# Performance work log

Measured on AMD Instinct MI355X. Metric: run time of the kernel, lower is better.

## Reference

```python
import jax, jax.numpy as jnp
import numpy as np

D_MODEL = 1024
N_HEADS = 16


def setup_inputs() -> dict:
    key = jax.random.key(0)
    ks = jax.random.split(key, 11)
    B, S, D = 2, 2048, D_MODEL
    scale = 1.0 / np.sqrt(D)
    inp = {
        "q": jax.random.normal(ks[0], (B, S, D), jnp.float32),
        "k": jax.random.normal(ks[1], (B, S, D), jnp.float32),
        "v": jax.random.normal(ks[2], (B, S, D), jnp.float32),
        "W_q": jax.random.normal(ks[3], (D, D), jnp.float32) * scale,
        "b_q": jnp.zeros((D,), jnp.float32),
        "W_k": jax.random.normal(ks[4], (D, D), jnp.float32) * scale,
        "b_k": jnp.zeros((D,), jnp.float32),
        "W_v": jax.random.normal(ks[5], (D, D), jnp.float32) * scale,
        "b_v": jnp.zeros((D,), jnp.float32),
        "W_o": jax.random.normal(ks[6], (D, D), jnp.float32) * scale,
        "b_o": jnp.zeros((D,), jnp.float32),
    }
    return inp


def reference(q, k, v, W_q, b_q, W_k, b_k, W_v, b_v, W_o, b_o):
    B, S, D = q.shape
    H = N_HEADS
    d_k = D // H
    # linear projections, then split heads: [B, H, S, d_k]
    def proj(x, W, b):
        y = jnp.einsum("bsd,de->bse", x, W.T) + b
        return y.reshape(B, S, H, d_k).transpose(0, 2, 1, 3)
    Q = proj(q, W_q, b_q)
    K = proj(k, W_k, b_k)
    V = proj(v, W_v, b_v)
    # scaled dot-product attention with explicit [B,H,S,S] scores
    scores = jnp.einsum("bhqd,bhkd->bhqk", Q, K) / jnp.sqrt(jnp.float32(d_k))
    attn = jax.nn.softmax(scores, axis=-1)
    out = jnp.einsum("bhqk,bhkd->bhqd", attn, V)
    out = out.transpose(0, 2, 1, 3).reshape(B, S, D)
    return jnp.einsum("bsd,de->bse", out, W_o.T) + b_o
```

## Files before the change

### kernel.cpp

```cpp
#include <hip/hip_runtime.h>
#include <hip/hip_bf16.h>
#include <math.h>

typedef __bf16 bf16_t;
typedef bf16_t bf16x8 __attribute__((ext_vector_type(8)));
typedef float f32x4 __attribute__((ext_vector_type(4)));

#define D_MODEL 1024
#define NH 16
#define DK 64
#define SEQ 2048
#define MROWS 4096
#define LDP 72
#define LDSW 64
#define LDC 136

__device__ __forceinline__ bf16x8 ldfrag(const bf16_t* p) {
    union { uint4 u; bf16x8 v; } c;
    c.u = *reinterpret_cast<const uint4*>(p);
    return c.v;
}

__device__ __forceinline__ f32x4 zero4() { f32x4 z = {0.f, 0.f, 0.f, 0.f}; return z; }

__device__ __forceinline__ void gll16(const bf16_t* g, bf16_t* l) {
    __builtin_amdgcn_global_load_lds(
        (const __attribute__((address_space(1))) unsigned int*)g,
        (__attribute__((address_space(3))) unsigned int*)l,
        16, 0, 0);
}

__global__ void pack3(const float* __restrict__ a, const float* __restrict__ b,
                      const float* __restrict__ c,
                      bf16_t* __restrict__ da, bf16_t* __restrict__ db, bf16_t* __restrict__ dc) {
    const float* s = (blockIdx.y == 0) ? a : (blockIdx.y == 1) ? b : c;
    bf16_t* d      = (blockIdx.y == 0) ? da : (blockIdx.y == 1) ? db : dc;
    int i = (blockIdx.x * blockDim.x + threadIdx.x) * 4;
    float4 f = *reinterpret_cast<const float4*>(s + i);
    union { bf16_t h[4]; uint2 u; } o;
    o.h[0] = (bf16_t)f.x; o.h[1] = (bf16_t)f.y; o.h[2] = (bf16_t)f.z; o.h[3] = (bf16_t)f.w;
    *reinterpret_cast<uint2*>(d + i) = o.u;
}

__global__ void pack4(const float* __restrict__ a, const float* __restrict__ b,
                      const float* __restrict__ c, const float* __restrict__ e,
                      bf16_t* __restrict__ da, bf16_t* __restrict__ db,
                      bf16_t* __restrict__ dc, bf16_t* __restrict__ de) {
    const float* s = (blockIdx.y == 0) ? a : (blockIdx.y == 1) ? b : (blockIdx.y == 2) ? c : e;
    bf16_t* d      = (blockIdx.y == 0) ? da : (blockIdx.y == 1) ? db : (blockIdx.y == 2) ? dc : de;
    int i = (blockIdx.x * blockDim.x + threadIdx.x) * 4;
    float4 f = *reinterpret_cast<const float4*>(s + i);
    union { bf16_t h[4]; uint2 u; } o;
    o.h[0] = (bf16_t)f.x; o.h[1] = (bf16_t)f.y; o.h[2] = (bf16_t)f.z; o.h[3] = (bf16_t)f.w;
    *reinterpret_cast<uint2*>(d + i) = o.u;
}

__device__ __forceinline__ void gemm_core(
    const bf16_t* __restrict__ A, const bf16_t* __restrict__ Bm,
    int K, int m0, int n0,
    bf16_t* As, bf16_t* Bs,
    f32x4 acc[4][4]) {

    const int tid = threadIdx.x;
    const int lane = tid & 63;
    const int wid = tid >> 6;
    const int wm = (wid >> 1) * 64, wn = (wid & 1) * 64;
    const int l15 = lane & 15, quad = lane >> 4;

    const int lrow   = lane >> 3;
    const int gcol   = ((lane & 7) ^ lrow) * 8;

    #pragma unroll
    for (int i = 0; i < 4; i++)
        #pragma unroll
        for (int j = 0; j < 4; j++) acc[i][j] = zero4();

    for (int k0 = 0; k0 < K; k0 += 64) {
        __syncthreads();
        #pragma unroll
        for (int t = 0; t < 4; t++) {
            const int rbase = wid * 32 + t * 8;
            gll16(A  + (size_t)(m0 + rbase + lrow) * K + k0 + gcol, As + rbase * LDSW);
            gll16(Bm + (size_t)(n0 + rbase + lrow) * K + k0 + gcol, Bs + rbase * LDSW);
        }
        __syncthreads();
        #pragma unroll
        for (int c = 0; c < 2; c++) {
            bf16x8 af[4], bfr[4];
            #pragma unroll
            for (int i = 0; i < 4; i++) {
                const int row = wm + i * 16 + l15;
                const int pc = ((c * 4 + quad) ^ (l15 & 7)) * 8;
                af[i] = ldfrag(As + row * LDSW + pc);
            }
            #pragma unroll
            for (int j = 0; j < 4; j++) {
                const int row = wn + j * 16 + l15;
                const int pc = ((c * 4 + quad) ^ (l15 & 7)) * 8;
                bfr[j] = ldfrag(Bs + row * LDSW + pc);
            }
            #pragma unroll
            for (int i = 0; i < 4; i++)
                #pragma unroll
                for (int j = 0; j < 4; j++)
                    acc[i][j] = __builtin_amdgcn_mfma_f32_16x16x32_bf16(af[i], bfr[j], acc[i][j], 0, 0, 0);
        }
    }
}

__global__ __launch_bounds__(256, 2) void proj_gemm(
    const bf16_t* __restrict__ qb, const bf16_t* __restrict__ kb,
    const bf16_t* __restrict__ vb,
    const bf16_t* __restrict__ Wq, const bf16_t* __restrict__ Wk,
    const bf16_t* __restrict__ Wv,
    const float* __restrict__ bq, const float* __restrict__ bk, const float* __restrict__ bv,
    bf16_t* __restrict__ Qh, bf16_t* __restrict__ Kh, bf16_t* __restrict__ Vt) {

    __shared__ __align__(16) bf16_t sm[128 * LDC];
    bf16_t* As = sm;
    bf16_t* Bs = sm + 128 * LDSW;
    bf16_t (*Cs)[LDC] = reinterpret_cast<bf16_t(*)[LDC]>(sm);
    f32x4 acc[4][4];

    const int mode = blockIdx.z;
    const bf16_t* X = (mode == 0) ? qb : (mode == 1) ? kb : vb;
    const bf16_t* W = (mode == 0) ? Wq : (mode == 1) ? Wk : Wv;
    const float* bias = (mode == 0) ? bq : (mode == 1) ? bk : bv;
    const int m0 = blockIdx.y * 128, n0 = blockIdx.x * 128;

    gemm_core(X, W, D_MODEL, m0, n0, As, Bs, acc);

    const int tid = threadIdx.x, lane = tid & 63, wid = tid >> 6;
    const int wm = (wid >> 1) * 64, wn = (wid & 1) * 64;
    const int l15 = lane & 15, quad = lane >> 4;

    __syncthreads();
    if (mode != 2) {
        const float sc = (mode == 0) ? 0.125f * 1.44269504f : 1.0f;
        #pragma unroll
        for (int i = 0; i < 4; i++)
            #pragma unroll
            for (int j = 0; j < 4; j++)
                #pragma unroll
                for (int r = 0; r < 4; r++) {
                    int gn = n0 + wn + j * 16 + l15;
                    Cs[wm + i * 16 + quad * 4 + r][wn + j * 16 + l15] =
                        (bf16_t)((acc[i][j][r] + bias[gn]) * sc);
                }
    } else {
        #pragma unroll
        for (int i = 0; i < 4; i++)
            #pragma unroll
            for (int j = 0; j < 4; j++)
                #pragma unroll
                for (int r = 0; r < 4; r++) {
                    int gn = n0 + wn + j * 16 + l15;
                    Cs[wn + j * 16 + l15][wm + i * 16 + quad * 4 + r] =
                        (bf16_t)(acc[i][j][r] + bias[gn]);
                }
    }
    __syncthreads();

    #pragma unroll
    for (int c = tid; c < 2048; c += 256) {
        int row = c >> 4, col8 = (c & 15) << 3;
        uint4 val = *reinterpret_cast<const uint4*>(&Cs[row][col8]);
        if (mode != 2) {
            int gm = m0 + row, gn = n0 + col8;
            int b = gm >> 11, seq = gm & 2047;
            int h = gn >> 6, dk = gn & 63;
            bf16_t* dst = (mode == 0) ? Qh : Kh;
            *reinterpret_cast<uint4*>(dst + ((size_t)(b * NH + h) * SEQ + seq) * DK + dk) = val;
        } else {
            int gn = n0 + row, gm = m0 + col8;
            int b = gm >> 11, seq = gm & 2047;
            int h = gn >> 6, dk = gn & 63;
            *reinterpret_cast<uint4*>(Vt + ((size_t)(b * NH + h) * DK + dk) * SEQ + seq) = val;
        }
    }
}

__global__ __launch_bounds__(256, 2) void out_gemm(
    const bf16_t* __restrict__ Oc, const bf16_t* __restrict__ Wo,
    const float* __restrict__ bo, float* __restrict__ Cout) {

    __shared__ __align__(16) bf16_t As[128 * LDSW];
    __shared__ __align__(16) bf16_t Bs[128 * LDSW];
    f32x4 acc[4][4];
    const int m0 = blockIdx.y * 128, n0 = blockIdx.x * 128;

    gemm_core(Oc, Wo, D_MODEL, m0, n0, As, Bs, acc);

    const int tid = threadIdx.x, lane = tid & 63, wid = tid >> 6;
    const int wm = (wid >> 1) * 64, wn = (wid & 1) * 64;
    const int l15 = lane & 15, quad = lane >> 4;

    #pragma unroll
    for (int i = 0; i < 4; i++)
        #pragma unroll
        for (int j = 0; j < 4; j++)
            #pragma unroll
            for (int r = 0; r < 4; r++) {
                int gm = m0 + wm + i * 16 + quad * 4 + r;
                int gn = n0 + wn + j * 16 + l15;
                Cout[(size_t)gm * D_MODEL + gn] = acc[i][j][r] + bo[gn];
            }
}

__global__ __launch_bounds__(256) void attn_kernel(
    const bf16_t* __restrict__ Qh, const bf16_t* __restrict__ Kh,
    const bf16_t* __restrict__ Vt, bf16_t* __restrict__ Oc) {

    __shared__ __align__(16) bf16_t Ks[64 * LDSW];
    __shared__ __align__(16) bf16_t Vts[64 * LDSW];
    __shared__ __align__(16) bf16_t Pls[64][LDP];

    const int tid = threadIdx.x, lane = tid & 63, wid = tid >> 6;
    const int l15 = lane & 15, quad = lane >> 4;
    const int bh = blockIdx.x;
    const int q0 = blockIdx.y * 64;
    const bf16_t* Qbase = Qh + (size_t)bh * SEQ * DK;
    const bf16_t* Kbase = Kh + (size_t)bh * SEQ * DK;
    const bf16_t* Vbase = Vt + (size_t)bh * DK * SEQ;

    const int lrow = lane >> 3;
    const int gcol = ((lane & 7) ^ lrow) * 8;

    bf16x8 aQ[2];
    #pragma unroll
    for (int c = 0; c < 2; c++)
        aQ[c] = ldfrag(Qbase + (size_t)(q0 + wid * 16 + l15) * DK + c * 32 + quad * 8);

    f32x4 oacc[4];
    #pragma unroll
    for (int j = 0; j < 4; j++) oacc[j] = zero4();
    float l_i[4] = {0.f, 0.f, 0.f, 0.f};

    for (int kt = 0; kt < SEQ / 64; kt++) {
        const int k0 = kt * 64;
        __syncthreads();
        #pragma unroll
        for (int t = 0; t < 2; t++) {
            const int rbase = wid * 16 + t * 8;
            gll16(Kbase + (size_t)(k0 + rbase + lrow) * DK + gcol,  Ks  + rbase * LDSW);
            gll16(Vbase + (size_t)(rbase + lrow) * SEQ + k0 + gcol, Vts + rbase * LDSW);
        }
        __syncthreads();

        f32x4 sacc[4];
        #pragma unroll
        for (int j = 0; j < 4; j++) sacc[j] = zero4();
        #pragma unroll
        for (int c = 0; c < 2; c++) {
            bf16x8 bk4[4];
            #pragma unroll
            for (int j = 0; j < 4; j++) {
                const int pc = ((c * 4 + quad) ^ (l15 & 7)) * 8;
                bk4[j] = ldfrag(Ks + (j * 16 + l15) * LDSW + pc);
            }
            #pragma unroll
            for (int j = 0; j < 4; j++)
                sacc[j] = __builtin_amdgcn_mfma_f32_16x16x32_bf16(
                    aQ[c], bk4[j], sacc[j], 0, 0, 0);
        }

        #pragma unroll
        for (int r = 0; r < 4; r++) {
            float e0 = exp2f(sacc[0][r]);
            float e1 = exp2f(sacc[1][r]);
            float e2 = exp2f(sacc[2][r]);
            float e3 = exp2f(sacc[3][r]);
            l_i[r] += (e0 + e1) + (e2 + e3);
            bf16_t* prow = &Pls[wid * 16 + quad * 4 + r][0];
            prow[l15]      = (bf16_t)e0;
            prow[16 + l15] = (bf16_t)e1;
            prow[32 + l15] = (bf16_t)e2;
            prow[48 + l15] = (bf16_t)e3;
        }

        #pragma unroll
        for (int c = 0; c < 2; c++) {
            bf16x8 ap = ldfrag(&Pls[wid * 16 + l15][c * 32 + quad * 8]);
            bf16x8 bv4[4];
            #pragma unroll
            for (int j = 0; j < 4; j++) {
                const int pc = ((c * 4 + quad) ^ (l15 & 7)) * 8;
                bv4[j] = ldfrag(Vts + (j * 16 + l15) * LDSW + pc);
            }
            #pragma unroll
            for (int j = 0; j < 4; j++)
                oacc[j] = __builtin_amdgcn_mfma_f32_16x16x32_bf16(
                    ap, bv4[j], oacc[j], 0, 0, 0);
        }
    }

    #pragma unroll
    for (int r = 0; r < 4; r++) {
        float l = l_i[r];
        #pragma unroll
        for (int off = 1; off < 16; off <<= 1)
            l += __shfl_xor(l, off, 64);
        float inv = 1.0f / l;
        #pragma unroll
        for (int j = 0; j < 4; j++)
            Pls[wid * 16 + quad * 4 + r][j * 16 + l15] = (bf16_t)(oacc[j][r] * inv);
    }
    __syncthreads();

    const int b = bh >> 4, h = bh & 15;
    #pragma unroll
    for (int c = tid; c < 512; c += 256) {
        int row = c >> 3, col8 = (c & 7) << 3;
        uint4 val = *reinterpret_cast<const uint4*>(&Pls[row][col8]);
        *reinterpret_cast<uint4*>(Oc + ((size_t)(b * SEQ + q0 + row)) * D_MODEL + h * DK + col8) = val;
    }
}

extern "C" void kernel_launch(void* const* d_in, const int* in_sizes, int n_in,
                              void* d_out, int out_size, void* d_ws, size_t ws_size,
                              hipStream_t stream) {
    const float* q  = (const float*)d_in[0];
    const float* k  = (const float*)d_in[1];
    const float* v  = (const float*)d_in[2];
    const float* Wq = (const float*)d_in[3];
    const float* bq = (const float*)d_in[4];
    const float* Wk = (const float*)d_in[5];
    const float* bk = (const float*)d_in[6];
    const float* Wv = (const float*)d_in[7];
    const float* bv = (const float*)d_in[8];
    const float* Wo = (const float*)d_in[9];
    const float* bo = (const float*)d_in[10];

    const size_t nx = (size_t)MROWS * D_MODEL;
    const size_t nw = (size_t)D_MODEL * D_MODEL;

    bf16_t* qb  = (bf16_t*)d_ws;
    bf16_t* kb  = qb  + nx;
    bf16_t* vb  = kb  + nx;
    bf16_t* Wqb = vb  + nx;
    bf16_t* Wkb = Wqb + nw;
    bf16_t* Wvb = Wkb + nw;
    bf16_t* Wob = Wvb + nw;
    bf16_t* Qh  = Wob + nw;
    bf16_t* Kh  = Qh  + nx;
    bf16_t* Vt  = Kh  + nx;
    bf16_t* Oc  = Vt  + nx;

    pack3<<<dim3(4096, 3), 256, 0, stream>>>(q, k, v, qb, kb, vb);
    pack4<<<dim3(1024, 4), 256, 0, stream>>>(Wq, Wk, Wv, Wo, Wqb, Wkb, Wvb, Wob);

    proj_gemm<<<dim3(8, 32, 3), 256, 0, stream>>>(qb, kb, vb, Wqb, Wkb, Wvb, bq, bk, bv, Qh, Kh, Vt);
    attn_kernel<<<dim3(32, 32), 256, 0, stream>>>(Qh, Kh, Vt, Oc);
    out_gemm<<<dim3(8, 32), 256, 0, stream>>>(Oc, Wob, bo, (float*)d_out);
}
```

Measured before the change: 248.7 us.

## Double-buffer K/V tiles in attention, swizzle P buffer, add MFMA priority

The attention kernel now double-buffers the K and V LDS tiles, issuing the async global-to-LDS load for the next tile before computing on the current one. It waits with a partial vmcnt and a single barrier per iteration instead of two syncthreads. The padded P scratch is replaced by an XOR-swizzled unpadded layout to avoid bank conflicts, and s_setprio raises wave priority around the MFMA blocks. This overlaps memory latency with compute, at the cost of doubling K/V LDS use and relying on exact waitcnt accounting.

Result: slower. 261.5 us (+5.1%).

```diff
diff --git a/kernel.cpp b/kernel.cpp
--- a/kernel.cpp
+++ b/kernel.cpp
@@ -11,7 +11,6 @@
 #define DK 64
 #define SEQ 2048
 #define MROWS 4096
-#define LDP 72
 #define LDSW 64
 #define LDC 136
 
@@ -211,9 +210,9 @@
     const bf16_t* __restrict__ Qh, const bf16_t* __restrict__ Kh,
     const bf16_t* __restrict__ Vt, bf16_t* __restrict__ Oc) {
 
-    __shared__ __align__(16) bf16_t Ks[64 * LDSW];
-    __shared__ __align__(16) bf16_t Vts[64 * LDSW];
-    __shared__ __align__(16) bf16_t Pls[64][LDP];
+    __shared__ __align__(16) bf16_t Ks[2][64 * LDSW];
+    __shared__ __align__(16) bf16_t Vts[2][64 * LDSW];
+    __shared__ __align__(16) bf16_t Pls[64 * LDSW];
 
     const int tid = threadIdx.x, lane = tid & 63, wid = tid >> 6;
     const int l15 = lane & 15, quad = lane >> 4;
@@ -236,33 +235,51 @@
     for (int j = 0; j < 4; j++) oacc[j] = zero4();
     float l_i[4] = {0.f, 0.f, 0.f, 0.f};
 
+    #pragma unroll
+    for (int t = 0; t < 2; t++) {
+        const int rbase = wid * 16 + t * 8;
+        gll16(Kbase + (size_t)(rbase + lrow) * DK + gcol,  Ks[0]  + rbase * LDSW);
+        gll16(Vbase + (size_t)(rbase + lrow) * SEQ + gcol, Vts[0] + rbase * LDSW);
+    }
+
+    const int pch = l15 >> 3, pwi = l15 & 7;
+
     for (int kt = 0; kt < SEQ / 64; kt++) {
-        const int k0 = kt * 64;
-        __syncthreads();
+        const int buf = kt & 1;
+        const int nkt = (kt + 1 < SEQ / 64) ? kt + 1 : kt;
+        const int nk0 = nkt * 64;
+
         #pragma unroll
         for (int t = 0; t < 2; t++) {
             const int rbase = wid * 16 + t * 8;
-            gll16(Kbase + (size_t)(k0 + rbase + lrow) * DK + gcol,  Ks  + rbase * LDSW);
-            gll16(Vbase + (size_t)(rbase + lrow) * SEQ + k0 + gcol, Vts + rbase * LDSW);
-        }
-        __syncthreads();
+            gll16(Kbase + (size_t)(nk0 + rbase + lrow) * DK + gcol,  Ks[buf ^ 1]  + rbase * LDSW);
+            gll16(Vbase + (size_t)(rbase + lrow) * SEQ + nk0 + gcol, Vts[buf ^ 1] + rbase * LDSW);
+        }
+        asm volatile("s_waitcnt vmcnt(4)" ::: "memory");
+        __builtin_amdgcn_s_barrier();
+        __builtin_amdgcn_sched_barrier(0);
+
+        const bf16_t* Kb = Ks[buf];
+        const bf16_t* Vb = Vts[buf];
 
         f32x4 sacc[4];
         #pragma unroll
         for (int j = 0; j < 4; j++) sacc[j] = zero4();
+        __builtin_amdgcn_s_setprio(1);
         #pragma unroll
         for (int c = 0; c < 2; c++) {
             bf16x8 bk4[4];
             #pragma unroll
             for (int j = 0; j < 4; j++) {
                 const int pc = ((c * 4 + quad) ^ (l15 & 7)) * 8;
-                bk4[j] = ldfrag(Ks + (j * 16 + l15) * LDSW + pc);
+                bk4[j] = ldfrag(Kb + (j * 16 + l15) * LDSW + pc);
             }
             #pragma unroll
             for (int j = 0; j < 4; j++)
                 sacc[j] = __builtin_amdgcn_mfma_f32_16x16x32_bf16(
                     aQ[c], bk4[j], sacc[j], 0, 0, 0);
         }
+        __builtin_amdgcn_s_setprio(0);
 
         #pragma unroll
         for (int r = 0; r < 4; r++) {
@@ -271,27 +288,33 @@
             float e2 = exp2f(sacc[2][r]);
             float e3 = exp2f(sacc[3][r]);
             l_i[r] += (e0 + e1) + (e2 + e3);
-            bf16_t* prow = &Pls[wid * 16 + quad * 4 + r][0];
-            prow[l15]      = (bf16_t)e0;
-            prow[16 + l15] = (bf16_t)e1;
-            prow[32 + l15] = (bf16_t)e2;
-            prow[48 + l15] = (bf16_t)e3;
-        }
-
+            bf16_t* prow = Pls + (wid * 16 + quad * 4 + r) * LDSW;
+            const int rx = (quad * 4 + r) & 7;
+            prow[((pch    ) ^ rx) * 8 + pwi] = (bf16_t)e0;
+            prow[((pch + 2) ^ rx) * 8 + pwi] = (bf16_t)e1;
+            prow[((pch + 4) ^ rx) * 8 + pwi] = (bf16_t)e2;
+            prow[((pch + 6) ^ rx) * 8 + pwi] = (bf16_t)e3;
+        }
+
+        __builtin_amdgcn_s_setprio(1);
         #pragma unroll
         for (int c = 0; c < 2; c++) {
-            bf16x8 ap = ldfrag(&Pls[wid * 16 + l15][c * 32 + quad * 8]);
+            bf16x8 ap = ldfrag(Pls + (wid * 16 + l15) * LDSW +
+                               (((c * 4 + quad) ^ (l15 & 7)) << 3));
             bf16x8 bv4[4];
             #pragma unroll
             for (int j = 0; j < 4; j++) {
                 const int pc = ((c * 4 + quad) ^ (l15 & 7)) * 8;
-                bv4[j] = ldfrag(Vts + (j * 16 + l15) * LDSW + pc);
+                bv4[j] = ldfrag(Vb + (j * 16 + l15) * LDSW + pc);
             }
             #pragma unroll
             for (int j = 0; j < 4; j++)
                 oacc[j] = __builtin_amdgcn_mfma_f32_16x16x32_bf16(
                     ap, bv4[j], oacc[j], 0, 0, 0);
         }
+        __builtin_amdgcn_s_setprio(0);
+
+        __builtin_amdgcn_s_barrier();
     }
 
     #pragma unroll
@@ -301,18 +324,21 @@
         for (int off = 1; off < 16; off <<= 1)
             l += __shfl_xor(l, off, 64);
         float inv = 1.0f / l;
+        bf16_t* prow = Pls + (wid * 16 + quad * 4 + r) * LDSW;
+        const int rx = (quad * 4 + r) & 7;
         #pragma unroll
         for (int j = 0; j < 4; j++)
-            Pls[wid * 16 + quad * 4 + r][j * 16 + l15] = (bf16_t)(oacc[j][r] * inv);
+            prow[((pch + 2 * j) ^ rx) * 8 + pwi] = (bf16_t)(oacc[j][r] * inv);
     }
     __syncthreads();
 
     const int b = bh >> 4, h = bh & 15;
     #pragma unroll
     for (int c = tid; c < 512; c += 256) {
-        int row = c >> 3, col8 = (c & 7) << 3;
-        uint4 val = *reinterpret_cast<const uint4*>(&Pls[row][col8]);
-        *reinterpret_cast<uint4*>(Oc + ((size_t)(b * SEQ + q0 + row)) * D_MODEL + h * DK + col8) = val;
+        int row = c >> 3, chunk = c & 7;
+        uint4 val = *reinterpret_cast<const uint4*>(
+            Pls + row * LDSW + ((chunk ^ (row & 7)) << 3));
+        *reinterpret_cast<uint4*>(Oc + ((size_t)(b * SEQ + q0 + row)) * D_MODEL + h * DK + (chunk << 3)) = val;
     }
 }
 
```

## Transpose QK^T MFMA operands so P is stored as packed 8-byte swizzled writes

Applied to the files above, without the earlier changes.

Swaps the MFMA operand order for the score computation so each lane holds four consecutive key columns of one query row. The P tile can then be written to LDS as packed 64-bit stores into an XOR-swizzled layout without padding, replacing 16 scalar bf16 stores. The row-sum reduction becomes two cross-quad shuffles instead of four butterfly stages per row. The output staging uses the same swizzle, which adds index arithmetic and an extra broadcast shuffle per row in the epilogue.

After: 242.8 us. -2.4%, faster.

```diff
diff --git a/kernel.cpp b/kernel.cpp
--- a/kernel.cpp
+++ b/kernel.cpp
@@ -11,7 +11,6 @@
 #define DK 64
 #define SEQ 2048
 #define MROWS 4096
-#define LDP 72
 #define LDSW 64
 #define LDC 136
 
@@ -213,7 +212,7 @@
 
     __shared__ __align__(16) bf16_t Ks[64 * LDSW];
     __shared__ __align__(16) bf16_t Vts[64 * LDSW];
-    __shared__ __align__(16) bf16_t Pls[64][LDP];
+    __shared__ __align__(16) bf16_t Pls[64 * LDSW];
 
     const int tid = threadIdx.x, lane = tid & 63, wid = tid >> 6;
     const int l15 = lane & 15, quad = lane >> 4;
@@ -234,7 +233,10 @@
     f32x4 oacc[4];
     #pragma unroll
     for (int j = 0; j < 4; j++) oacc[j] = zero4();
-    float l_i[4] = {0.f, 0.f, 0.f, 0.f};
+    float l_acc = 0.f;
+
+    const int s7 = l15 & 7;
+    bf16_t* prow = Pls + (wid * 16 + l15) * LDSW;
 
     for (int kt = 0; kt < SEQ / 64; kt++) {
         const int k0 = kt * 64;
@@ -255,36 +257,37 @@
             bf16x8 bk4[4];
             #pragma unroll
             for (int j = 0; j < 4; j++) {
-                const int pc = ((c * 4 + quad) ^ (l15 & 7)) * 8;
+                const int pc = ((c * 4 + quad) ^ s7) * 8;
                 bk4[j] = ldfrag(Ks + (j * 16 + l15) * LDSW + pc);
             }
             #pragma unroll
             for (int j = 0; j < 4; j++)
                 sacc[j] = __builtin_amdgcn_mfma_f32_16x16x32_bf16(
-                    aQ[c], bk4[j], sacc[j], 0, 0, 0);
-        }
-
-        #pragma unroll
-        for (int r = 0; r < 4; r++) {
-            float e0 = exp2f(sacc[0][r]);
-            float e1 = exp2f(sacc[1][r]);
-            float e2 = exp2f(sacc[2][r]);
-            float e3 = exp2f(sacc[3][r]);
-            l_i[r] += (e0 + e1) + (e2 + e3);
-            bf16_t* prow = &Pls[wid * 16 + quad * 4 + r][0];
-            prow[l15]      = (bf16_t)e0;
-            prow[16 + l15] = (bf16_t)e1;
-            prow[32 + l15] = (bf16_t)e2;
-            prow[48 + l15] = (bf16_t)e3;
+                    bk4[j], aQ[c], sacc[j], 0, 0, 0);
+        }
+
+        #pragma unroll
+        for (int j = 0; j < 4; j++) {
+            float e0 = exp2f(sacc[j][0]);
+            float e1 = exp2f(sacc[j][1]);
+            float e2 = exp2f(sacc[j][2]);
+            float e3 = exp2f(sacc[j][3]);
+            l_acc += (e0 + e1) + (e2 + e3);
+            union { bf16_t h[4]; unsigned long long u; } pk;
+            pk.h[0] = (bf16_t)e0; pk.h[1] = (bf16_t)e1;
+            pk.h[2] = (bf16_t)e2; pk.h[3] = (bf16_t)e3;
+            const int Lc = j * 2 + (quad >> 1);
+            *reinterpret_cast<unsigned long long*>(
+                prow + ((Lc ^ s7) << 3) + ((quad & 1) << 2)) = pk.u;
         }
 
         #pragma unroll
         for (int c = 0; c < 2; c++) {
-            bf16x8 ap = ldfrag(&Pls[wid * 16 + l15][c * 32 + quad * 8]);
+            bf16x8 ap = ldfrag(prow + (((c * 4 + quad) ^ s7) << 3));
             bf16x8 bv4[4];
             #pragma unroll
             for (int j = 0; j < 4; j++) {
-                const int pc = ((c * 4 + quad) ^ (l15 & 7)) * 8;
+                const int pc = ((c * 4 + quad) ^ s7) * 8;
                 bv4[j] = ldfrag(Vts + (j * 16 + l15) * LDSW + pc);
             }
             #pragma unroll
@@ -294,25 +297,30 @@
         }
     }
 
+    float l = l_acc;
+    l += __shfl_xor(l, 16, 64);
+    l += __shfl_xor(l, 32, 64);
+
+    const int pch = l15 >> 3, pwi = l15 & 7;
     #pragma unroll
     for (int r = 0; r < 4; r++) {
-        float l = l_i[r];
-        #pragma unroll
-        for (int off = 1; off < 16; off <<= 1)
-            l += __shfl_xor(l, off, 64);
-        float inv = 1.0f / l;
+        float lr = __shfl(l, quad * 4 + r, 16);
+        float inv = 1.0f / lr;
+        bf16_t* orow = Pls + (wid * 16 + quad * 4 + r) * LDSW;
+        const int rx = (quad * 4 + r) & 7;
         #pragma unroll
         for (int j = 0; j < 4; j++)
-            Pls[wid * 16 + quad * 4 + r][j * 16 + l15] = (bf16_t)(oacc[j][r] * inv);
+            orow[((pch + 2 * j) ^ rx) * 8 + pwi] = (bf16_t)(oacc[j][r] * inv);
     }
     __syncthreads();
 
     const int b = bh >> 4, h = bh & 15;
     #pragma unroll
     for (int c = tid; c < 512; c += 256) {
-        int row = c >> 3, col8 = (c & 7) << 3;
-        uint4 val = *reinterpret_cast<const uint4*>(&Pls[row][col8]);
-        *reinterpret_cast<uint4*>(Oc + ((size_t)(b * SEQ + q0 + row)) * D_MODEL + h * DK + col8) = val;
+        int row = c >> 3, chunk = c & 7;
+        uint4 val = *reinterpret_cast<const uint4*>(
+            Pls + row * LDSW + ((chunk ^ (row & 7)) << 3));
+        *reinterpret_cast<uint4*>(Oc + ((size_t)(b * SEQ + q0 + row)) * D_MODEL + h * DK + (chunk << 3)) = val;
     }
 }
 
```
